# Kernel optimization log

Hardware: AMD Instinct MI355X
Metric: run time of the kernel (lower is better)

Reference implementation:

```python
import jax, jax.numpy as jnp
import numpy as np

N_NODES = 50000


def _sage_conv(x, src, dst, Wl, bl, Wr):
    # mean aggregation of source-node features into target nodes
    agg = jax.ops.segment_sum(x[src], dst, num_segments=N_NODES)      # [N, C]
    deg = jax.ops.segment_sum(jnp.ones_like(src, dtype=x.dtype), dst,
                              num_segments=N_NODES)                   # [N]
    mean = agg / jnp.maximum(deg, 1.0)[:, None]
    # PyG SAGEConv: lin_l(aggr) (with bias) + lin_r(x) (no bias)
    return mean @ Wl.T + bl + x @ Wr.T


def setup_inputs() -> dict:
    key = jax.random.key(0)
    ks = jax.random.split(key, 8)
    C = 128
    E = 600000
    scale = 1.0 / np.sqrt(C)
    x = jax.random.normal(ks[0], (N_NODES, C), dtype=jnp.float32)
    edge_index = jax.random.randint(ks[1], (2, E), 0, N_NODES, dtype=jnp.int64)
    Wl1 = jax.random.normal(ks[2], (C, C), dtype=jnp.float32) * scale
    bl1 = jnp.zeros((C,), dtype=jnp.float32)
    Wr1 = jax.random.normal(ks[3], (C, C), dtype=jnp.float32) * scale
    Wl2 = jax.random.normal(ks[4], (C, C), dtype=jnp.float32) * scale
    bl2 = jnp.zeros((C,), dtype=jnp.float32)
    Wr2 = jax.random.normal(ks[5], (C, C), dtype=jnp.float32) * scale
    return {"x": x, "edge_index": edge_index, "Wl1": Wl1, "bl1": bl1,
            "Wr1": Wr1, "Wl2": Wl2, "bl2": bl2, "Wr2": Wr2}


def reference(x, edge_index, Wl1, bl1, Wr1, Wl2, bl2, Wr2):
    src, dst = edge_index[0], edge_index[1]
    h = _sage_conv(x, src, dst, Wl1, bl1, Wr1)
    h = jax.nn.relu(h)
    out = _sage_conv(h, src, dst, Wl2, bl2, Wr2)
    return out
```

## Files before the change

kernel.cpp:

```cpp
#include <hip/hip_runtime.h>
#include <hip/hip_bf16.h>

#define N_NODES 50000
#define C 128
#define NPAD 50176
#define FB_ROWS 16
#define FUSED_BLOCKS (N_NODES / FB_ROWS)
#define XPREP_BLOCKS 3125
#define WPREP_BLOCKS 256
#define CAP 48
#define CSTRIDE 32
#define FPITCH 132

typedef short bf16x8 __attribute__((ext_vector_type(8)));
typedef float f32x4 __attribute__((ext_vector_type(4)));

__device__ __forceinline__ unsigned short f2bf(float f) {
    unsigned int u = __float_as_uint(f);
    unsigned int r = u + 0x7fffu + ((u >> 16) & 1u);
    return (unsigned short)(r >> 16);
}

__device__ __forceinline__ float bf2f(unsigned short b) {
    return __uint_as_float(((unsigned int)b) << 16);
}

__device__ __forceinline__ void acc8(float* a, uint4 u) {
    const unsigned int uu[4] = {u.x, u.y, u.z, u.w};
#pragma unroll
    for (int i = 0; i < 4; ++i) {
        a[2 * i] += bf2f((unsigned short)uu[i]);
        a[2 * i + 1] += bf2f((unsigned short)(uu[i] >> 16));
    }
}

__global__ __launch_bounds__(256) void buildfill_kernel(
    const int* __restrict__ src, const int* __restrict__ dst, int E, int edgeBlocks,
    int* __restrict__ cursor, int* __restrict__ csr,
    const float* __restrict__ x, unsigned short* __restrict__ Xb,
    const float* __restrict__ Wl1, const float* __restrict__ Wr1,
    const float* __restrict__ Wl2, const float* __restrict__ Wr2,
    unsigned short* __restrict__ Wc1, unsigned short* __restrict__ Wc2) {
    int b = blockIdx.x;
    if (b < edgeBlocks) {
        int e = b * 256 + threadIdx.x;
        if (e < E) {
            int d = dst[e];
            int s = src[e];
            if ((unsigned)d < (unsigned)N_NODES && (unsigned)s < (unsigned)N_NODES) {
                int slot = atomicAdd(cursor + d * CSTRIDE, 1);
                if (slot < CAP) csr[d * CAP + slot] = s;
            }
        }
    } else if (b < edgeBlocks + XPREP_BLOCKS) {
        int t = (b - edgeBlocks) * 256 + threadIdx.x;
        if (t >= N_NODES * C / 8) return;
        const float4 a = *(const float4*)(x + (size_t)t * 8);
        const float4 c = *(const float4*)(x + (size_t)t * 8 + 4);
        unsigned short o[8] = {f2bf(a.x), f2bf(a.y), f2bf(a.z), f2bf(a.w),
                               f2bf(c.x), f2bf(c.y), f2bf(c.z), f2bf(c.w)};
        *(uint4*)(Xb + (size_t)t * 8) = *(const uint4*)o;
    } else {
        int idx = (b - edgeBlocks - XPREP_BLOCKS) * 256 + threadIdx.x;
        int layer = idx >> 15;
        int r = idx & 32767;
        int j = r >> 8, k = r & 255;
        const float* Wl = layer ? Wl2 : Wl1;
        const float* Wr = layer ? Wr2 : Wr1;
        unsigned short* Wc = layer ? Wc2 : Wc1;
        float f = (k < 128) ? Wl[j * 128 + k] : Wr[j * 128 + (k - 128)];
        Wc[r] = f2bf(f);
    }
}

__global__ __launch_bounds__(256, 4) void sage_fused16(
    const unsigned short* __restrict__ feat,
    const int* __restrict__ cursor, const int* __restrict__ csr,
    const unsigned short* __restrict__ Wc,
    const float* __restrict__ bias,
    void* __restrict__ outv, int relu, int obf16) {
    __shared__ unsigned short fm[FB_ROWS * FPITCH];

    const int lane = threadIdx.x & 63;
    const int w = threadIdx.x >> 6;
    const int g = lane >> 4;
    const int c = lane & 15;
    const int base = blockIdx.x * FB_ROWS;
    const unsigned short* fp = feat + c * 8;

    const int n0 = base + w * 4;
    int degr[4], idx[4];
#pragma unroll
    for (int i = 0; i < 4; ++i) degr[i] = cursor[(size_t)(n0 + i) * CSTRIDE];
#pragma unroll
    for (int i = 0; i < 4; ++i) idx[i] = (lane < CAP) ? csr[(n0 + i) * CAP + lane] : 0;

#pragma unroll
    for (int p = 0; p < 2; ++p) {
        const int d0 = min(degr[2 * p], CAP);
        const int d1 = min(degr[2 * p + 1], CAP);
        const int i0 = idx[2 * p], i1 = idx[2 * p + 1];
        const int nb0 = (d0 + 3) >> 2, nb1 = (d1 + 3) >> 2;
        uint4 u0[6], u1[6];
#pragma unroll
        for (int b = 0; b < 6; ++b) {
            if (b < nb0) {
                int r = 4 * b + g;
                int s = __shfl(i0, r < d0 ? r : 0);
                u0[b] = *(const uint4*)(fp + (size_t)s * C);
            }
        }
#pragma unroll
        for (int b = 0; b < 6; ++b) {
            if (b < nb1) {
                int r = 4 * b + g;
                int s = __shfl(i1, r < d1 ? r : 0);
                u1[b] = *(const uint4*)(fp + (size_t)s * C);
            }
        }
        float a[8];
#pragma unroll
        for (int k = 0; k < 8; ++k) a[k] = 0.f;
#pragma unroll
        for (int b = 0; b < 6; ++b)
            if (b < nb0 && 4 * b + g < d0) acc8(a, u0[b]);
        if (nb0 > 6) {
            for (int b = 6; b < nb0; ++b) {
                int r = 4 * b + g;
                int s = __shfl(i0, r < d0 ? r : 0);
                uint4 uu = *(const uint4*)(fp + (size_t)s * C);
                if (r < d0) acc8(a, uu);
            }
        }
#pragma unroll
        for (int k = 0; k < 8; ++k) {
            a[k] += __shfl_xor(a[k], 16);
            a[k] += __shfl_xor(a[k], 32);
        }
        {
            const float inv = 1.0f / fmaxf((float)d0, 1.0f);
            if (g == 0) {
                unsigned int o[4];
#pragma unroll
                for (int k = 0; k < 4; ++k)
                    o[k] = (unsigned)f2bf(a[2 * k] * inv) |
                           ((unsigned)f2bf(a[2 * k + 1] * inv) << 16);
                *(uint4*)(&fm[(w * 4 + 2 * p) * FPITCH + c * 8]) = *(const uint4*)o;
            }
        }
#pragma unroll
        for (int k = 0; k < 8; ++k) a[k] = 0.f;
#pragma unroll
        for (int b = 0; b < 6; ++b)
            if (b < nb1 && 4 * b + g < d1) acc8(a, u1[b]);
        if (nb1 > 6) {
            for (int b = 6; b < nb1; ++b) {
                int r = 4 * b + g;
                int s = __shfl(i1, r < d1 ? r : 0);
                uint4 uu = *(const uint4*)(fp + (size_t)s * C);
                if (r < d1) acc8(a, uu);
            }
        }
#pragma unroll
        for (int k = 0; k < 8; ++k) {
            a[k] += __shfl_xor(a[k], 16);
            a[k] += __shfl_xor(a[k], 32);
        }
        {
            const float inv = 1.0f / fmaxf((float)d1, 1.0f);
            if (g == 0) {
                unsigned int o[4];
#pragma unroll
                for (int k = 0; k < 4; ++k)
                    o[k] = (unsigned)f2bf(a[2 * k] * inv) |
                           ((unsigned)f2bf(a[2 * k + 1] * inv) << 16);
                *(uint4*)(&fm[(w * 4 + 2 * p + 1) * FPITCH + c * 8]) = *(const uint4*)o;
            }
        }
    }
    __syncthreads();

    if (w != 0) return;
    const int m = lane & 15;
    const int q = lane >> 4;
    const unsigned short* as = feat + (size_t)(base + m) * C + q * 8;

    f32x4 acc[8];
#pragma unroll
    for (int j = 0; j < 8; ++j) acc[j] = (f32x4){0.f, 0.f, 0.f, 0.f};

#pragma unroll
    for (int kt = 0; kt < 8; ++kt) {
        bf16x8 af;
        if (kt < 4)
            af = *(const bf16x8*)(&fm[m * FPITCH + kt * 32 + q * 8]);
        else
            af = *(const bf16x8*)(as + (kt & 3) * 32);
#pragma unroll
        for (int jt = 0; jt < 8; ++jt) {
            bf16x8 bfrag = *(const bf16x8*)(Wc + (jt * 16 + m) * 256 + kt * 32 + q * 8);
            acc[jt] = __builtin_amdgcn_mfma_f32_16x16x32_bf16(af, bfrag, acc[jt], 0, 0, 0);
        }
    }

    const int rbase = base + q * 4;
#pragma unroll
    for (int r = 0; r < 4; ++r) {
        int row = rbase + r;
#pragma unroll
        for (int jt = 0; jt < 8; ++jt) {
            int col = jt * 16 + m;
            float v = acc[jt][r] + bias[col];
            if (relu) v = fmaxf(v, 0.0f);
            if (obf16)
                ((unsigned short*)outv)[(size_t)row * C + col] = f2bf(v);
            else
                ((float*)outv)[(size_t)row * C + col] = v;
        }
    }
}

extern "C" void kernel_launch(void* const* d_in, const int* in_sizes, int n_in,
                              void* d_out, int out_size, void* d_ws, size_t ws_size,
                              hipStream_t stream) {
    const float* x = (const float*)d_in[0];
    const int* edge = (const int*)d_in[1];
    const float* Wl1 = (const float*)d_in[2];
    const float* bl1 = (const float*)d_in[3];
    const float* Wr1 = (const float*)d_in[4];
    const float* Wl2 = (const float*)d_in[5];
    const float* bl2 = (const float*)d_in[6];
    const float* Wr2 = (const float*)d_in[7];
    float* out = (float*)d_out;

    const int E = in_sizes[1] / 2;
    const int* src = edge;
    const int* dst = edge + E;

    char* ws = (char*)d_ws;
    size_t off = 0;
    int* cursor = (int*)(ws + off);           off += (size_t)N_NODES * CSTRIDE * 4;
    off = (off + 511) & ~511ull;
    int* csr = (int*)(ws + off);              off += (size_t)N_NODES * CAP * 4;
    off = (off + 511) & ~511ull;
    unsigned short* Xb = (unsigned short*)(ws + off); off += (size_t)NPAD * C * 2;
    unsigned short* h  = (unsigned short*)(ws + off); off += (size_t)NPAD * C * 2;
    unsigned short* Wc1 = (unsigned short*)(ws + off); off += 128 * 256 * 2;
    unsigned short* Wc2 = (unsigned short*)(ws + off); off += 128 * 256 * 2;
    (void)ws_size;

    const int edgeBlocks = (E + 255) / 256;

    hipMemsetAsync(cursor, 0, (size_t)N_NODES * CSTRIDE * 4, stream);
    buildfill_kernel<<<edgeBlocks + XPREP_BLOCKS + WPREP_BLOCKS, 256, 0, stream>>>(
        src, dst, E, edgeBlocks, cursor, csr, x, Xb, Wl1, Wr1, Wl2, Wr2, Wc1, Wc2);

    sage_fused16<<<FUSED_BLOCKS, 256, 0, stream>>>(Xb, cursor, csr, Wc1, bl1, h, 1, 1);

    sage_fused16<<<FUSED_BLOCKS, 256, 0, stream>>>(h, cursor, csr, Wc2, bl2, out, 0, 0);
}
```

Baseline: 209.8 us.

## Merge build and both SAGE layers into one persistent kernel with grid barriers

Replaces the memset, the build/convert kernel and the two per-layer kernels with a single persistent kernel of 1024 blocks. The phases are separated by atomic-counter grid barriers, and the cursor array is zeroed inside the kernel. The MFMA stage now spreads its output columns over all four waves instead of running on wave 0 alone. This removes launch gaps and the idle waves in the GEMM tail, but it relies on all 1024 blocks being co-resident for the barrier and serialises the phases behind spin-waits.

```diff
diff --git a/kernel.cpp b/kernel.cpp
--- a/kernel.cpp
+++ b/kernel.cpp
@@ -1,16 +1,13 @@
 #include <hip/hip_runtime.h>
-#include <hip/hip_bf16.h>
 
 #define N_NODES 50000
 #define C 128
-#define NPAD 50176
 #define FB_ROWS 16
-#define FUSED_BLOCKS (N_NODES / FB_ROWS)
-#define XPREP_BLOCKS 3125
-#define WPREP_BLOCKS 256
+#define NTILE (N_NODES / FB_ROWS)
 #define CAP 48
 #define CSTRIDE 32
 #define FPITCH 132
+#define GRID_BLOCKS 1024
 
 typedef short bf16x8 __attribute__((ext_vector_type(8)));
 typedef float f32x4 __attribute__((ext_vector_type(4)));
@@ -34,36 +31,199 @@
     }
 }
 
-__global__ __launch_bounds__(256) void buildfill_kernel(
-    const int* __restrict__ src, const int* __restrict__ dst, int E, int edgeBlocks,
+__device__ __forceinline__ void grid_bar(int* bar, int target) {
+    __syncthreads();
+    if (threadIdx.x == 0) {
+        __threadfence();
+        __hip_atomic_fetch_add(bar, 1, __ATOMIC_RELEASE, __HIP_MEMORY_SCOPE_AGENT);
+        while (__hip_atomic_load(bar, __ATOMIC_RELAXED, __HIP_MEMORY_SCOPE_AGENT) < target)
+            __builtin_amdgcn_s_sleep(8);
+        __threadfence();
+    }
+    __syncthreads();
+}
+
+__device__ __forceinline__ void layer_pass(
+    const unsigned short* __restrict__ feat,
+    const int* __restrict__ cursor, const int* __restrict__ csr,
+    const unsigned short* __restrict__ Wc,
+    const float* __restrict__ bias,
+    void* __restrict__ outv, int relu, int obf16,
+    unsigned short* fm) {
+    const int lane = threadIdx.x & 63;
+    const int w = threadIdx.x >> 6;
+    const int g = lane >> 4;
+    const int c = lane & 15;
+    const unsigned short* fp = feat + c * 8;
+
+    for (int tile = blockIdx.x; tile < NTILE; tile += gridDim.x) {
+        const int base = tile * FB_ROWS;
+        const int n0 = base + w * 4;
+        int degr[4], idx[4];
+#pragma unroll
+        for (int i = 0; i < 4; ++i) degr[i] = cursor[(size_t)(n0 + i) * CSTRIDE];
+#pragma unroll
+        for (int i = 0; i < 4; ++i) idx[i] = (lane < CAP) ? csr[(n0 + i) * CAP + lane] : 0;
+
+#pragma unroll
+        for (int p = 0; p < 2; ++p) {
+            const int d0 = min(degr[2 * p], CAP);
+            const int d1 = min(degr[2 * p + 1], CAP);
+            const int i0 = idx[2 * p], i1 = idx[2 * p + 1];
+            const int nb0 = (d0 + 3) >> 2, nb1 = (d1 + 3) >> 2;
+            uint4 u0[6], u1[6];
+#pragma unroll
+            for (int b = 0; b < 6; ++b) {
+                if (b < nb0) {
+                    int r = 4 * b + g;
+                    int s = __shfl(i0, r < d0 ? r : 0);
+                    u0[b] = *(const uint4*)(fp + (size_t)s * C);
+                }
+            }
+#pragma unroll
+            for (int b = 0; b < 6; ++b) {
+                if (b < nb1) {
+                    int r = 4 * b + g;
+                    int s = __shfl(i1, r < d1 ? r : 0);
+                    u1[b] = *(const uint4*)(fp + (size_t)s * C);
+                }
+            }
+            float a[8];
+#pragma unroll
+            for (int k = 0; k < 8; ++k) a[k] = 0.f;
+#pragma unroll
+            for (int b = 0; b < 6; ++b)
+                if (b < nb0 && 4 * b + g < d0) acc8(a, u0[b]);
+            if (nb0 > 6) {
+                for (int b = 6; b < nb0; ++b) {
+                    int r = 4 * b + g;
+                    int s = __shfl(i0, r < d0 ? r : 0);
+                    uint4 uu = *(const uint4*)(fp + (size_t)s * C);
+                    if (r < d0) acc8(a, uu);
+                }
+            }
+#pragma unroll
+            for (int k = 0; k < 8; ++k) {
+                a[k] += __shfl_xor(a[k], 16);
+                a[k] += __shfl_xor(a[k], 32);
+            }
+            {
+                const float inv = 1.0f / fmaxf((float)d0, 1.0f);
+                if (g == 0) {
+                    unsigned int o[4];
+#pragma unroll
+                    for (int k = 0; k < 4; ++k)
+                        o[k] = (unsigned)f2bf(a[2 * k] * inv) |
+                               ((unsigned)f2bf(a[2 * k + 1] * inv) << 16);
+                    *(uint4*)(&fm[(w * 4 + 2 * p) * FPITCH + c * 8]) = *(const uint4*)o;
+                }
+            }
+#pragma unroll
+            for (int k = 0; k < 8; ++k) a[k] = 0.f;
+#pragma unroll
+            for (int b = 0; b < 6; ++b)
+                if (b < nb1 && 4 * b + g < d1) acc8(a, u1[b]);
+            if (nb1 > 6) {
+                for (int b = 6; b < nb1; ++b) {
+                    int r = 4 * b + g;
+                    int s = __shfl(i1, r < d1 ? r : 0);
+                    uint4 uu = *(const uint4*)(fp + (size_t)s * C);
+                    if (r < d1) acc8(a, uu);
+                }
+            }
+#pragma unroll
+            for (int k = 0; k < 8; ++k) {
+                a[k] += __shfl_xor(a[k], 16);
+                a[k] += __shfl_xor(a[k], 32);
+            }
+            {
+                const float inv = 1.0f / fmaxf((float)d1, 1.0f);
+                if (g == 0) {
+                    unsigned int o[4];
+#pragma unroll
+                    for (int k = 0; k < 4; ++k)
+                        o[k] = (unsigned)f2bf(a[2 * k] * inv) |
+                               ((unsigned)f2bf(a[2 * k + 1] * inv) << 16);
+                    *(uint4*)(&fm[(w * 4 + 2 * p + 1) * FPITCH + c * 8]) = *(const uint4*)o;
+                }
+            }
+        }
+        __syncthreads();
+
+        const unsigned short* as = feat + (size_t)(base + c) * C + g * 8;
+        f32x4 acc2[2];
+        acc2[0] = (f32x4){0.f, 0.f, 0.f, 0.f};
+        acc2[1] = (f32x4){0.f, 0.f, 0.f, 0.f};
+#pragma unroll
+        for (int kt = 0; kt < 8; ++kt) {
+            bf16x8 af;
+            if (kt < 4)
+                af = *(const bf16x8*)(&fm[c * FPITCH + kt * 32 + g * 8]);
+            else
+                af = *(const bf16x8*)(as + (kt & 3) * 32);
+#pragma unroll
+            for (int j = 0; j < 2; ++j) {
+                bf16x8 bfrag = *(const bf16x8*)(Wc + ((w * 2 + j) * 16 + c) * 256 + kt * 32 + g * 8);
+                acc2[j] = __builtin_amdgcn_mfma_f32_16x16x32_bf16(af, bfrag, acc2[j], 0, 0, 0);
+            }
+        }
+#pragma unroll
+        for (int j = 0; j < 2; ++j) {
+            const int col = (w * 2 + j) * 16 + c;
+            const float bcol = bias[col];
+#pragma unroll
+            for (int r = 0; r < 4; ++r) {
+                const int row = base + g * 4 + r;
+                float v = acc2[j][r] + bcol;
+                if (relu) v = fmaxf(v, 0.0f);
+                if (obf16)
+                    ((unsigned short*)outv)[(size_t)row * C + col] = f2bf(v);
+                else
+                    ((float*)outv)[(size_t)row * C + col] = v;
+            }
+        }
+        __syncthreads();
+    }
+}
+
+__global__ __launch_bounds__(256, 4) void sage_mega(
+    const int* __restrict__ src, const int* __restrict__ dst, int E,
     int* __restrict__ cursor, int* __restrict__ csr,
     const float* __restrict__ x, unsigned short* __restrict__ Xb,
     const float* __restrict__ Wl1, const float* __restrict__ Wr1,
     const float* __restrict__ Wl2, const float* __restrict__ Wr2,
-    unsigned short* __restrict__ Wc1, unsigned short* __restrict__ Wc2) {
-    int b = blockIdx.x;
-    if (b < edgeBlocks) {
-        int e = b * 256 + threadIdx.x;
-        if (e < E) {
-            int d = dst[e];
-            int s = src[e];
-            if ((unsigned)d < (unsigned)N_NODES && (unsigned)s < (unsigned)N_NODES) {
-                int slot = atomicAdd(cursor + d * CSTRIDE, 1);
-                if (slot < CAP) csr[d * CAP + slot] = s;
-            }
-        }
-    } else if (b < edgeBlocks + XPREP_BLOCKS) {
-        int t = (b - edgeBlocks) * 256 + threadIdx.x;
-        if (t >= N_NODES * C / 8) return;
+    unsigned short* __restrict__ Wc1, unsigned short* __restrict__ Wc2,
+    const float* __restrict__ bl1, const float* __restrict__ bl2,
+    unsigned short* __restrict__ h, float* __restrict__ out,
+    int* __restrict__ bar) {
+    __shared__ unsigned short fm[FB_ROWS * FPITCH];
+    const int nthr = gridDim.x * 256;
+    const int tid = blockIdx.x * 256 + threadIdx.x;
+
+    {
+        const uint4 z = {0u, 0u, 0u, 0u};
+        for (int i = tid; i < N_NODES * CSTRIDE / 4; i += nthr)
+            ((uint4*)cursor)[i] = z;
+    }
+    grid_bar(bar, GRID_BLOCKS * 1);
+
+    for (int e = tid; e < E; e += nthr) {
+        int d = dst[e], s = src[e];
+        if ((unsigned)d < (unsigned)N_NODES && (unsigned)s < (unsigned)N_NODES) {
+            int slot = atomicAdd(cursor + d * CSTRIDE, 1);
+            if (slot < CAP) csr[d * CAP + slot] = s;
+        }
+    }
+    for (int t = tid; t < N_NODES * C / 8; t += nthr) {
         const float4 a = *(const float4*)(x + (size_t)t * 8);
-        const float4 c = *(const float4*)(x + (size_t)t * 8 + 4);
+        const float4 c2 = *(const float4*)(x + (size_t)t * 8 + 4);
         unsigned short o[8] = {f2bf(a.x), f2bf(a.y), f2bf(a.z), f2bf(a.w),
-                               f2bf(c.x), f2bf(c.y), f2bf(c.z), f2bf(c.w)};
+                               f2bf(c2.x), f2bf(c2.y), f2bf(c2.z), f2bf(c2.w)};
         *(uint4*)(Xb + (size_t)t * 8) = *(const uint4*)o;
-    } else {
-        int idx = (b - edgeBlocks - XPREP_BLOCKS) * 256 + threadIdx.x;
-        int layer = idx >> 15;
-        int r = idx & 32767;
+    }
+    for (int t = tid; t < 65536; t += nthr) {
+        int layer = t >> 15;
+        int r = t & 32767;
         int j = r >> 8, k = r & 255;
         const float* Wl = layer ? Wl2 : Wl1;
         const float* Wr = layer ? Wr2 : Wr1;
@@ -71,153 +231,12 @@
         float f = (k < 128) ? Wl[j * 128 + k] : Wr[j * 128 + (k - 128)];
         Wc[r] = f2bf(f);
     }
-}
-
-__global__ __launch_bounds__(256, 4) void sage_fused16(
-    const unsigned short* __restrict__ feat,
-    const int* __restrict__ cursor, const int* __restrict__ csr,
-    const unsigned short* __restrict__ Wc,
-    const float* __restrict__ bias,
-    void* __restrict__ outv, int relu, int obf16) {
-    __shared__ unsigned short fm[FB_ROWS * FPITCH];
-
-    const int lane = threadIdx.x & 63;
-    const int w = threadIdx.x >> 6;
-    const int g = lane >> 4;
-    const int c = lane & 15;
-    const int base = blockIdx.x * FB_ROWS;
-    const unsigned short* fp = feat + c * 8;
-
-    const int n0 = base + w * 4;
-    int degr[4], idx[4];
-#pragma unroll
-    for (int i = 0; i < 4; ++i) degr[i] = cursor[(size_t)(n0 + i) * CSTRIDE];
-#pragma unroll
-    for (int i = 0; i < 4; ++i) idx[i] = (lane < CAP) ? csr[(n0 + i) * CAP + lane] : 0;
-
-#pragma unroll
-    for (int p = 0; p < 2; ++p) {
-        const int d0 = min(degr[2 * p], CAP);
-        const int d1 = min(degr[2 * p + 1], CAP);
-        const int i0 = idx[2 * p], i1 = idx[2 * p + 1];
-        const int nb0 = (d0 + 3) >> 2, nb1 = (d1 + 3) >> 2;
-        uint4 u0[6], u1[6];
-#pragma unroll
-        for (int b = 0; b < 6; ++b) {
-            if (b < nb0) {
-                int r = 4 * b + g;
-                int s = __shfl(i0, r < d0 ? r : 0);
-                u0[b] = *(const uint4*)(fp + (size_t)s * C);
-            }
-        }
-#pragma unroll
-        for (int b = 0; b < 6; ++b) {
-            if (b < nb1) {
-                int r = 4 * b + g;
-                int s = __shfl(i1, r < d1 ? r : 0);
-                u1[b] = *(const uint4*)(fp + (size_t)s * C);
-            }
-        }
-        float a[8];
-#pragma unroll
-        for (int k = 0; k < 8; ++k) a[k] = 0.f;
-#pragma unroll
-        for (int b = 0; b < 6; ++b)
-            if (b < nb0 && 4 * b + g < d0) acc8(a, u0[b]);
-        if (nb0 > 6) {
-            for (int b = 6; b < nb0; ++b) {
-                int r = 4 * b + g;
-                int s = __shfl(i0, r < d0 ? r : 0);
-                uint4 uu = *(const uint4*)(fp + (size_t)s * C);
-                if (r < d0) acc8(a, uu);
-            }
-        }
-#pragma unroll
-        for (int k = 0; k < 8; ++k) {
-            a[k] += __shfl_xor(a[k], 16);
-            a[k] += __shfl_xor(a[k], 32);
-        }
-        {
-            const float inv = 1.0f / fmaxf((float)d0, 1.0f);
-            if (g == 0) {
-                unsigned int o[4];
-#pragma unroll
-                for (int k = 0; k < 4; ++k)
-                    o[k] = (unsigned)f2bf(a[2 * k] * inv) |
-                           ((unsigned)f2bf(a[2 * k + 1] * inv) << 16);
-                *(uint4*)(&fm[(w * 4 + 2 * p) * FPITCH + c * 8]) = *(const uint4*)o;
-            }
-        }
-#pragma unroll
-        for (int k = 0; k < 8; ++k) a[k] = 0.f;
-#pragma unroll
-        for (int b = 0; b < 6; ++b)
-            if (b < nb1 && 4 * b + g < d1) acc8(a, u1[b]);
-        if (nb1 > 6) {
-            for (int b = 6; b < nb1; ++b) {
-                int r = 4 * b + g;
-                int s = __shfl(i1, r < d1 ? r : 0);
-                uint4 uu = *(const uint4*)(fp + (size_t)s * C);
-                if (r < d1) acc8(a, uu);
-            }
-        }
-#pragma unroll
-        for (int k = 0; k < 8; ++k) {
-            a[k] += __shfl_xor(a[k], 16);
-            a[k] += __shfl_xor(a[k], 32);
-        }
-        {
-            const float inv = 1.0f / fmaxf((float)d1, 1.0f);
-            if (g == 0) {
-                unsigned int o[4];
-#pragma unroll
-                for (int k = 0; k < 4; ++k)
-                    o[k] = (unsigned)f2bf(a[2 * k] * inv) |
-                           ((unsigned)f2bf(a[2 * k + 1] * inv) << 16);
-                *(uint4*)(&fm[(w * 4 + 2 * p + 1) * FPITCH + c * 8]) = *(const uint4*)o;
-            }
-        }
-    }
-    __syncthreads();
-
-    if (w != 0) return;
-    const int m = lane & 15;
-    const int q = lane >> 4;
-    const unsigned short* as = feat + (size_t)(base + m) * C + q * 8;
-
-    f32x4 acc[8];
-#pragma unroll
-    for (int j = 0; j < 8; ++j) acc[j] = (f32x4){0.f, 0.f, 0.f, 0.f};
-
-#pragma unroll
-    for (int kt = 0; kt < 8; ++kt) {
-        bf16x8 af;
-        if (kt < 4)
-            af = *(const bf16x8*)(&fm[m * FPITCH + kt * 32 + q * 8]);
-        else
-            af = *(const bf16x8*)(as + (kt & 3) * 32);
-#pragma unroll
-        for (int jt = 0; jt < 8; ++jt) {
-            bf16x8 bfrag = *(const bf16x8*)(Wc + (jt * 16 + m) * 256 + kt * 32 + q * 8);
-            acc[jt] = __builtin_amdgcn_mfma_f32_16x16x32_bf16(af, bfrag, acc[jt], 0, 0, 0);
-        }
-    }
-
-    const int rbase = base + q * 4;
-#pragma unroll
-    for (int r = 0; r < 4; ++r) {
-        int row = rbase + r;
-#pragma unroll
-        for (int jt = 0; jt < 8; ++jt) {
-            int col = jt * 16 + m;
-            float v = acc[jt][r] + bias[col];
-            if (relu) v = fmaxf(v, 0.0f);
-            if (obf16)
-                ((unsigned short*)outv)[(size_t)row * C + col] = f2bf(v);
-            else
-                ((float*)outv)[(size_t)row * C + col] = v;
-        }
-    }
+    grid_bar(bar, GRID_BLOCKS * 2);
+
+    layer_pass(Xb, cursor, csr, Wc1, bl1, h, 1, 1, fm);
+    grid_bar(bar, GRID_BLOCKS * 3);
+
+    layer_pass(h, cursor, csr, Wc2, bl2, out, 0, 0, fm);
 }
 
 extern "C" void kernel_launch(void* const* d_in, const int* in_sizes, int n_in,
@@ -233,29 +252,25 @@
     const float* Wr2 = (const float*)d_in[7];
     float* out = (float*)d_out;
 
-    const int E = in_sizes[1] / 2;
+    int E = in_sizes[1] / 2;
     const int* src = edge;
     const int* dst = edge + E;
 
     char* ws = (char*)d_ws;
     size_t off = 0;
+    int* bar = (int*)(ws + off);              off += 512;
     int* cursor = (int*)(ws + off);           off += (size_t)N_NODES * CSTRIDE * 4;
     off = (off + 511) & ~511ull;
     int* csr = (int*)(ws + off);              off += (size_t)N_NODES * CAP * 4;
     off = (off + 511) & ~511ull;
-    unsigned short* Xb = (unsigned short*)(ws + off); off += (size_t)NPAD * C * 2;
-    unsigned short* h  = (unsigned short*)(ws + off); off += (size_t)NPAD * C * 2;
+    unsigned short* Xb = (unsigned short*)(ws + off); off += (size_t)N_NODES * C * 2;
+    unsigned short* h  = (unsigned short*)(ws + off); off += (size_t)N_NODES * C * 2;
     unsigned short* Wc1 = (unsigned short*)(ws + off); off += 128 * 256 * 2;
     unsigned short* Wc2 = (unsigned short*)(ws + off); off += 128 * 256 * 2;
     (void)ws_size;
 
-    const int edgeBlocks = (E + 255) / 256;
-
-    hipMemsetAsync(cursor, 0, (size_t)N_NODES * CSTRIDE * 4, stream);
-    buildfill_kernel<<<edgeBlocks + XPREP_BLOCKS + WPREP_BLOCKS, 256, 0, stream>>>(
-        src, dst, E, edgeBlocks, cursor, csr, x, Xb, Wl1, Wr1, Wl2, Wr2, Wc1, Wc2);
-
-    sage_fused16<<<FUSED_BLOCKS, 256, 0, stream>>>(Xb, cursor, csr, Wc1, bl1, h, 1, 1);
-
-    sage_fused16<<<FUSED_BLOCKS, 256, 0, stream>>>(h, cursor, csr, Wc2, bl2, out, 0, 0);
-}
+    hipMemsetAsync(bar, 0, 512, stream);
+    sage_mega<<<GRID_BLOCKS, 256, 0, stream>>>(
+        src, dst, E, cursor, csr, x, Xb, Wl1, Wr1, Wl2, Wr2, Wc1, Wc2,
+        bl1, bl2, h, out, bar);
+}
```

Result: slower. 630.7 us (+200.6%).
